# Optimization experiments

Measured on AMD Instinct MI355X. Metric: run time of the kernel, lower is better.

Reference implementation:

```python
import jax, jax.numpy as jnp
import numpy as np

B, S, H = 2, 2048, 1024
NH, NKV, HD = 16, 4, 64
G, R = NKV, NH // NKV  # 4 kv groups, 4 query heads per group


def setup_inputs() -> dict:
    key = jax.random.key(0)
    ks = jax.random.split(key, 7)
    scale = 1.0 / np.sqrt(H)
    return {
        "hidden_states": jax.random.normal(ks[0], (B, S, H), jnp.float32),
        "cos": jax.random.normal(ks[1], (S, HD), jnp.float32),
        "sin": jax.random.normal(ks[2], (S, HD), jnp.float32),
        "attention_mask": jnp.ones((B, S), jnp.float32),
        "Wq": jax.random.normal(ks[3], (H, NH * HD), jnp.float32) * scale,
        "Wk": jax.random.normal(ks[4], (H, NKV * HD), jnp.float32) * scale,
        "Wv": jax.random.normal(ks[5], (H, NKV * HD), jnp.float32) * scale,
        "Wo": jax.random.normal(ks[6], (NH * HD, H), jnp.float32) * scale,
    }


def _rotate_half(x):
    h = x.shape[-1] // 2
    return jnp.concatenate([-x[..., h:], x[..., :h]], axis=-1)


def reference(hidden_states, cos, sin, attention_mask, Wq, Wk, Wv, Wo):
    x = hidden_states
    q = (x @ Wq).reshape(B, S, NH, HD)
    k = (x @ Wk).reshape(B, S, NKV, HD)
    v = (x @ Wv).reshape(B, S, NKV, HD)
    # RoPE: cos/sin [S,HD] broadcast over batch and heads
    c = cos[None, :, None, :]
    s = sin[None, :, None, :]
    q = q * c + _rotate_half(q) * s
    k = k * c + _rotate_half(k) * s
    # GQA without materializing repeated KV: q grouped as [B,S,G,R,HD]
    qg = q.reshape(B, S, G, R, HD)
    scores = jnp.einsum("bsgrd,btgd->bgrst", qg, k) / np.sqrt(HD)  # [B,G,R,S,T]
    causal = jnp.tril(jnp.ones((S, S), bool))
    scores = jnp.where(causal[None, None, None], scores, -jnp.inf)
    scores = scores + ((1.0 - attention_mask) * -1e9)[:, None, None, None, :]
    probs = jax.nn.softmax(scores.astype(jnp.float32), axis=-1).astype(q.dtype)
    out = jnp.einsum("bgrst,btgd->bsgrd", probs, v).reshape(B, S, NH * HD)
    return out @ Wo
```

## Files before the change

kernel.cpp:

```cpp
#include <hip/hip_runtime.h>
#include <math.h>

#define B_   2
#define S_   2048
#define H_   1024
#define NH_  16
#define NKV_ 4
#define HD_  64
#define R_   (NH_ / NKV_)
#define QKVW 1536

typedef __attribute__((ext_vector_type(8))) short bf16x8;
typedef __attribute__((ext_vector_type(4))) float f32x4;

__device__ inline short f2bf(float f) {
    unsigned u = __float_as_uint(f);
    u += 0x7FFF + ((u >> 16) & 1);
    return (short)(u >> 16);
}

__device__ inline void gload_lds16(const void* gptr, void* lptr) {
    __builtin_amdgcn_global_load_lds(
        (const __attribute__((address_space(1))) unsigned int*)gptr,
        (__attribute__((address_space(3))) unsigned int*)lptr,
        16, 0, 0);
}

__global__ __launch_bounds__(256) void tconv_all(const float* __restrict__ Wq,
                                                 const float* __restrict__ Wk,
                                                 const float* __restrict__ Wv,
                                                 const float* __restrict__ Wo,
                                                 short* __restrict__ Wqkvt,
                                                 short* __restrict__ Wot) {
    __shared__ short T[64][68];
    const int bx = blockIdx.x;
    const float* W; short* Wt; int N, idx;
    if (bx < 256)      { W = Wq; Wt = Wqkvt;                     N = 1024; idx = bx; }
    else if (bx < 320) { W = Wk; Wt = Wqkvt + 1024 * 1024;       N = 256;  idx = bx - 256; }
    else if (bx < 384) { W = Wv; Wt = Wqkvt + 1280 * 1024;       N = 256;  idx = bx - 320; }
    else               { W = Wo; Wt = Wot;                       N = 1024; idx = bx - 384; }
    const int ntiles = N >> 6;
    const int n0 = (idx % ntiles) * 64;
    const int k0 = (idx / ntiles) * 64;

    const int tid = threadIdx.x;
    const int r  = tid >> 4;
    const int c4 = (tid & 15) * 4;
#pragma unroll
    for (int t = 0; t < 4; t++) {
        int row = t * 16 + r;
        float4 v = *(const float4*)&W[(size_t)(k0 + row) * N + n0 + c4];
        T[c4 + 0][row] = f2bf(v.x);
        T[c4 + 1][row] = f2bf(v.y);
        T[c4 + 2][row] = f2bf(v.z);
        T[c4 + 3][row] = f2bf(v.w);
    }
    __syncthreads();
#pragma unroll
    for (int t = 0; t < 4; t++) {
        int row = t * 16 + r;
        short4 o = *(short4*)&T[row][c4];
        *(short4*)&Wt[(size_t)(n0 + row) * 1024 + k0 + c4] = o;
    }
}

__global__ __launch_bounds__(256) void gemm1_fused(const float* __restrict__ x,
                                                   const short* __restrict__ Bt,
                                                   short* __restrict__ qkv,
                                                   short* __restrict__ Vtg,
                                                   const float* __restrict__ cosb,
                                                   const float* __restrict__ sinb) {
    __shared__ short Ah[64 * 32];
    __shared__ short Bh[128 * 32];

    const int tid  = threadIdx.x;
    const int w    = tid >> 6;
    const int lane = tid & 63;
    const int ln   = lane & 15;
    const int qd   = lane >> 4;
    const int wr   = w >> 1, wc = w & 1;
    const int row0 = blockIdx.y * 64;
    const int col0 = blockIdx.x * 128;

    const int sr = lane >> 2;
    const int sk = (lane & 3) * 8;
    const int ar  = tid >> 2;
    const int ac8 = (tid & 3) * 8;

    f32x4 acc[2][4];
#pragma unroll
    for (int mi = 0; mi < 2; mi++)
#pragma unroll
        for (int ni = 0; ni < 4; ni++)
            acc[mi][ni] = (f32x4){0.f, 0.f, 0.f, 0.f};

    for (int k0 = 0; k0 < 1024; k0 += 32) {
        __syncthreads();
        {
            const float* xp = x + (size_t)(row0 + ar) * H_ + k0 + ac8;
            float4 a = *(const float4*)xp;
            float4 b2 = *(const float4*)(xp + 4);
            bf16x8 o;
            o[0] = f2bf(a.x);  o[1] = f2bf(a.y);  o[2] = f2bf(a.z);  o[3] = f2bf(a.w);
            o[4] = f2bf(b2.x); o[5] = f2bf(b2.y); o[6] = f2bf(b2.z); o[7] = f2bf(b2.w);
            *(bf16x8*)&Ah[ar * 32 + ac8] = o;
        }
        gload_lds16(Bt + (size_t)(col0 + w * 32 + sr) * 1024 + k0 + sk, &Bh[(w * 32) * 32]);
        gload_lds16(Bt + (size_t)(col0 + w * 32 + 16 + sr) * 1024 + k0 + sk, &Bh[(w * 32 + 16) * 32]);
        __syncthreads();

        bf16x8 af[2], bfr[4];
#pragma unroll
        for (int mi = 0; mi < 2; mi++)
            af[mi] = *(const bf16x8*)&Ah[(wr * 32 + mi * 16 + ln) * 32 + qd * 8];
#pragma unroll
        for (int ni = 0; ni < 4; ni++)
            bfr[ni] = *(const bf16x8*)&Bh[(wc * 64 + ni * 16 + ln) * 32 + qd * 8];
#pragma unroll
        for (int mi = 0; mi < 2; mi++)
#pragma unroll
            for (int ni = 0; ni < 4; ni++)
                acc[mi][ni] = __builtin_amdgcn_mfma_f32_16x16x32_bf16(af[mi], bfr[ni], acc[mi][ni], 0, 0, 0);
    }

    const int colw = col0 + wc * 64;
    if (colw < H_ + NKV_ * HD_) {
#pragma unroll
        for (int mi = 0; mi < 2; mi++)
#pragma unroll
            for (int i = 0; i < 4; i++) {
                const int row  = row0 + wr * 32 + mi * 16 + qd * 4 + i;
                const int spos = row & (S_ - 1);
                const float* cp = cosb + (size_t)spos * HD_;
                const float* sp = sinb + (size_t)spos * HD_;
                float o0[4];
#pragma unroll
                for (int ni = 0; ni < 2; ni++) {
                    const int d = ni * 16 + ln;
                    float x0 = acc[mi][ni][i], x1 = acc[mi][ni + 2][i];
                    o0[ni]     = x0 * cp[d]      - x1 * sp[d];
                    o0[ni + 2] = x1 * cp[d + 32] + x0 * sp[d + 32];
                }
                short* Cp = qkv + (size_t)row * QKVW + colw + ln;
#pragma unroll
                for (int ni = 0; ni < 4; ni++) Cp[ni * 16] = f2bf(o0[ni]);
            }
    } else {
        const int g = (colw - (H_ + NKV_ * HD_)) >> 6;
#pragma unroll
        for (int mi = 0; mi < 2; mi++) {
            const int rbase = row0 + wr * 32 + mi * 16 + qd * 4;
            const int bg = ((rbase >> 11) * NKV_) + g;
            const int s0 = rbase & (S_ - 1);
#pragma unroll
            for (int ni = 0; ni < 4; ni++) {
                const int d = ni * 16 + ln;
                short4 pk = { f2bf(acc[mi][ni][0]), f2bf(acc[mi][ni][1]),
                              f2bf(acc[mi][ni][2]), f2bf(acc[mi][ni][3]) };
                *(short4*)&Vtg[((size_t)bg * HD_ + d) * S_ + s0] = pk;
            }
        }
    }
}

__global__ __launch_bounds__(256) void gemm2_bt(const short* __restrict__ A, int lda,
                                                const short* __restrict__ Bt,
                                                float* __restrict__ C, int ldc,
                                                int K) {
    __shared__ short Ah[64 * 32];
    __shared__ short Bh[128 * 32];

    const int tid  = threadIdx.x;
    const int w    = tid >> 6;
    const int lane = tid & 63;
    const int ln   = lane & 15;
    const int qd   = lane >> 4;
    const int wr   = w >> 1, wc = w & 1;
    const int row0 = blockIdx.y * 64;
    const int col0 = blockIdx.x * 128;

    const int sr = lane >> 2;
    const int sk = (lane & 3) * 8;

    f32x4 acc[2][4];
#pragma unroll
    for (int mi = 0; mi < 2; mi++)
#pragma unroll
        for (int ni = 0; ni < 4; ni++)
            acc[mi][ni] = (f32x4){0.f, 0.f, 0.f, 0.f};

    for (int k0 = 0; k0 < K; k0 += 32) {
        __syncthreads();
        gload_lds16(A + (size_t)(row0 + w * 16 + sr) * lda + k0 + sk, &Ah[(w * 16) * 32]);
        gload_lds16(Bt + (size_t)(col0 + w * 32 + sr) * K + k0 + sk, &Bh[(w * 32) * 32]);
        gload_lds16(Bt + (size_t)(col0 + w * 32 + 16 + sr) * K + k0 + sk, &Bh[(w * 32 + 16) * 32]);
        __syncthreads();

        bf16x8 af[2], bfr[4];
#pragma unroll
        for (int mi = 0; mi < 2; mi++)
            af[mi] = *(const bf16x8*)&Ah[(wr * 32 + mi * 16 + ln) * 32 + qd * 8];
#pragma unroll
        for (int ni = 0; ni < 4; ni++)
            bfr[ni] = *(const bf16x8*)&Bh[(wc * 64 + ni * 16 + ln) * 32 + qd * 8];
#pragma unroll
        for (int mi = 0; mi < 2; mi++)
#pragma unroll
            for (int ni = 0; ni < 4; ni++)
                acc[mi][ni] = __builtin_amdgcn_mfma_f32_16x16x32_bf16(af[mi], bfr[ni], acc[mi][ni], 0, 0, 0);
    }

#pragma unroll
    for (int mi = 0; mi < 2; mi++)
#pragma unroll
        for (int i = 0; i < 4; i++) {
            const size_t row = row0 + wr * 32 + mi * 16 + qd * 4 + i;
            float* Cp = C + row * ldc + col0 + wc * 64 + ln;
#pragma unroll
            for (int ni = 0; ni < 4; ni++) Cp[ni * 16] = acc[mi][ni][i];
        }
}

__global__ __launch_bounds__(256) void attn_kernel(short* __restrict__ qkv,
                                                   const short* __restrict__ Vtg,
                                                   const float* __restrict__ maskb) {
    const int tid  = threadIdx.x;
    const int w    = tid >> 6;
    const int lane = tid & 63;
    const int ln   = lane & 15;
    const int qd   = lane >> 4;

    const int fid = blockIdx.x;
    const int bg  = fid & 7;
    const int u   = fid >> 3;
    const int b   = bg >> 2;
    const int g   = bg & 3;
    const int h   = g * R_ + (u & 3);
    const int a   = u >> 2;

    __shared__ short Ps[4][32 * 72];
    short* const ps = Ps[w];

    const short* const Kb = qkv + H_ + g * HD_;

    for (int half = 0; half < 2; half++) {
        const int qt   = half ? (15 - a) : a;
        const int ws   = half ? (3 - w) : w;
        const int rowb = qt * 128 + ws * 32;
        const int nt   = (rowb >> 6) + 1;

        bf16x8 qf[2][2];
#pragma unroll
        for (int rg = 0; rg < 2; rg++) {
            const short* qp = qkv + (size_t)(b * S_ + rowb + rg * 16 + ln) * QKVW + h * HD_;
            qf[rg][0] = *(const bf16x8*)&qp[qd * 8];
            qf[rg][1] = *(const bf16x8*)&qp[32 + qd * 8];
        }

        f32x4 O[2][4] = {};
        float mrow[2] = {-1e30f, -1e30f};
        float lrow[2] = {0.0f, 0.0f};

        for (int kt = 0; kt < nt; kt++) {
            const int base = kt * 64;

            bf16x8 ka0[4], ka1[4];
#pragma unroll
            for (int kg = 0; kg < 4; kg++) {
                const short* kp = Kb + (size_t)(b * S_ + base + kg * 16 + ln) * QKVW;
                ka0[kg] = *(const bf16x8*)&kp[qd * 8];
                ka1[kg] = *(const bf16x8*)&kp[32 + qd * 8];
            }
            bf16x8 vb[2][4];
#pragma unroll
            for (int kc2 = 0; kc2 < 2; kc2++)
#pragma unroll
                for (int dt = 0; dt < 4; dt++)
                    vb[kc2][dt] = *(const bf16x8*)
                        &Vtg[((size_t)bg * HD_ + dt * 16 + ln) * S_ + base + kc2 * 32 + qd * 8];

            float mt[4][4];
#pragma unroll
            for (int kg = 0; kg < 4; kg++) {
                float4 mv = *(const float4*)&maskb[b * S_ + base + kg * 16 + qd * 4];
                mt[kg][0] = (1.0f - mv.x) * -1e9f;
                mt[kg][1] = (1.0f - mv.y) * -1e9f;
                mt[kg][2] = (1.0f - mv.z) * -1e9f;
                mt[kg][3] = (1.0f - mv.w) * -1e9f;
            }

            f32x4 St[2][4];
#pragma unroll
            for (int kg = 0; kg < 4; kg++) {
#pragma unroll
                for (int rg = 0; rg < 2; rg++) {
                    f32x4 z = {0.f, 0.f, 0.f, 0.f};
                    z = __builtin_amdgcn_mfma_f32_16x16x32_bf16(ka0[kg], qf[rg][0], z, 0, 0, 0);
                    St[rg][kg] = __builtin_amdgcn_mfma_f32_16x16x32_bf16(ka1[kg], qf[rg][1], z, 0, 0, 0);
                }
            }

            const bool diag = (kt == nt - 1);

#pragma unroll
            for (int rg = 0; rg < 2; rg++) {
                const int qrow = rowb + rg * 16 + ln;
                float sc[4][4];
#pragma unroll
                for (int kg = 0; kg < 4; kg++) {
                    const int keyb = base + kg * 16 + qd * 4;
#pragma unroll
                    for (int i = 0; i < 4; i++) {
                        float v = fmaf(St[rg][kg][i], 0.125f, mt[kg][i]);
                        sc[kg][i] = (diag && (keyb + i > qrow)) ? -1e30f : v;
                    }
                }
                float mx = sc[0][0];
#pragma unroll
                for (int kg = 0; kg < 4; kg++)
#pragma unroll
                    for (int i = 0; i < 4; i++) mx = fmaxf(mx, sc[kg][i]);
                mx = fmaxf(mx, __shfl_xor(mx, 16));
                mx = fmaxf(mx, __shfl_xor(mx, 32));

                if (__ballot(mx > mrow[rg] + 8.0f)) {
                    float nm    = fmaxf(mrow[rg], mx);
                    float alpha = __expf(mrow[rg] - nm);
                    lrow[rg] *= alpha;
#pragma unroll
                    for (int i = 0; i < 4; i++) {
                        float av = __shfl(alpha, qd * 4 + i);
#pragma unroll
                        for (int dt = 0; dt < 4; dt++) O[rg][dt][i] *= av;
                    }
                    mrow[rg] = nm;
                }
                const float nm = mrow[rg];

                float ls = 0.0f;
                float pr[4][4];
#pragma unroll
                for (int kg = 0; kg < 4; kg++)
#pragma unroll
                    for (int i = 0; i < 4; i++) {
                        float p = __expf(sc[kg][i] - nm);
                        pr[kg][i] = p;
                        ls += p;
                    }
                ls += __shfl_xor(ls, 16);
                ls += __shfl_xor(ls, 32);
                lrow[rg] += ls;

#pragma unroll
                for (int kg = 0; kg < 4; kg++) {
                    short4 pk = { f2bf(pr[kg][0]), f2bf(pr[kg][1]),
                                  f2bf(pr[kg][2]), f2bf(pr[kg][3]) };
                    *(short4*)&ps[(rg * 16 + ln) * 72 + kg * 16 + qd * 4] = pk;
                }
            }

#pragma unroll
            for (int kc2 = 0; kc2 < 2; kc2++) {
                bf16x8 pa0 = *(const bf16x8*)&ps[(ln)      * 72 + kc2 * 32 + qd * 8];
                bf16x8 pa1 = *(const bf16x8*)&ps[(16 + ln) * 72 + kc2 * 32 + qd * 8];
#pragma unroll
                for (int dt = 0; dt < 4; dt++) {
                    O[0][dt] = __builtin_amdgcn_mfma_f32_16x16x32_bf16(pa0, vb[kc2][dt], O[0][dt], 0, 0, 0);
                    O[1][dt] = __builtin_amdgcn_mfma_f32_16x16x32_bf16(pa1, vb[kc2][dt], O[1][dt], 0, 0, 0);
                }
            }
        }

#pragma unroll
        for (int rg = 0; rg < 2; rg++)
#pragma unroll
            for (int i = 0; i < 4; i++) {
                float li  = __shfl(lrow[rg], qd * 4 + i);
                float inv = 1.0f / li;
                const int row = rowb + rg * 16 + qd * 4 + i;
                short* op = qkv + (size_t)(b * S_ + row) * QKVW + h * HD_ + ln;
#pragma unroll
                for (int dt = 0; dt < 4; dt++) op[dt * 16] = f2bf(O[rg][dt][i] * inv);
            }
    }
}

extern "C" void kernel_launch(void* const* d_in, const int* in_sizes, int n_in,
                              void* d_out, int out_size, void* d_ws, size_t ws_size,
                              hipStream_t stream) {
    const float* x     = (const float*)d_in[0];
    const float* cosb  = (const float*)d_in[1];
    const float* sinb  = (const float*)d_in[2];
    const float* maskb = (const float*)d_in[3];
    const float* Wq    = (const float*)d_in[4];
    const float* Wk    = (const float*)d_in[5];
    const float* Wv    = (const float*)d_in[6];
    const float* Wo    = (const float*)d_in[7];

    const int M = B_ * S_;

    short* qkv   = (short*)d_ws;
    short* Wqkvt = qkv + (size_t)M * QKVW;
    short* Wot   = Wqkvt + (size_t)QKVW * H_;
    short* Vtg   = Wot + (size_t)H_ * H_;
    float* out   = (float*)d_out;

    dim3 blk(256);

    tconv_all<<<dim3(640), blk, 0, stream>>>(Wq, Wk, Wv, Wo, Wqkvt, Wot);

    gemm1_fused<<<dim3(QKVW / 128, M / 64), blk, 0, stream>>>(x, Wqkvt, qkv, Vtg, cosb, sinb);

    attn_kernel<<<dim3(256), blk, 0, stream>>>(qkv, Vtg, maskb);

    gemm2_bt<<<dim3(H_ / 128, M / 64), blk, 0, stream>>>(qkv, QKVW, Wot, out, H_, H_);
}
```

Before: 204.3 us.

## Split attention into 16-row query strips with double-buffered KV prefetch

Each wave now owns a 16-row query strip instead of 32 rows. The launch grows to 512 blocks with launch_bounds(256,2), so more waves are in flight and causal work is balanced by pairing strip j with strip 127-j. The K and V fragments for the next tile are loaded into a second register set while the current tile is computed, which hides global-load latency. The cost is that each loaded K/V tile is reused by half as many query rows, roughly doubling K/V traffic, and the double buffers add register pressure.

```diff
diff --git a/kernel.cpp b/kernel.cpp
--- a/kernel.cpp
+++ b/kernel.cpp
@@ -221,9 +221,9 @@
         }
 }
 
-__global__ __launch_bounds__(256) void attn_kernel(short* __restrict__ qkv,
-                                                   const short* __restrict__ Vtg,
-                                                   const float* __restrict__ maskb) {
+__global__ __launch_bounds__(256, 2) void attn_kernel(short* __restrict__ qkv,
+                                                      const short* __restrict__ Vtg,
+                                                      const float* __restrict__ maskb) {
     const int tid  = threadIdx.x;
     const int w    = tid >> 6;
     const int lane = tid & 63;
@@ -236,152 +236,163 @@
     const int b   = bg >> 2;
     const int g   = bg & 3;
     const int h   = g * R_ + (u & 3);
-    const int a   = u >> 2;
-
-    __shared__ short Ps[4][32 * 72];
+    const int t   = u >> 2;
+    const int j0  = t * 4 + w;
+
+    __shared__ short Ps[4][16 * 72];
     short* const ps = Ps[w];
 
-    const short* const Kb = qkv + H_ + g * HD_;
-
-    for (int half = 0; half < 2; half++) {
-        const int qt   = half ? (15 - a) : a;
-        const int ws   = half ? (3 - w) : w;
-        const int rowb = qt * 128 + ws * 32;
-        const int nt   = (rowb >> 6) + 1;
-
-        bf16x8 qf[2][2];
-#pragma unroll
-        for (int rg = 0; rg < 2; rg++) {
-            const short* qp = qkv + (size_t)(b * S_ + rowb + rg * 16 + ln) * QKVW + h * HD_;
-            qf[rg][0] = *(const bf16x8*)&qp[qd * 8];
-            qf[rg][1] = *(const bf16x8*)&qp[32 + qd * 8];
-        }
-
-        f32x4 O[2][4] = {};
-        float mrow[2] = {-1e30f, -1e30f};
-        float lrow[2] = {0.0f, 0.0f};
-
-        for (int kt = 0; kt < nt; kt++) {
-            const int base = kt * 64;
-
-            bf16x8 ka0[4], ka1[4];
+    const short* const Kb = qkv + (size_t)b * S_ * QKVW + H_ + g * HD_;
+    const short* const Vb = Vtg + (size_t)bg * HD_ * S_;
+    const float* const mb = maskb + b * S_;
+
+#pragma unroll 1
+    for (int ss = 0; ss < 2; ss++) {
+        const int j    = ss ? (127 - j0) : j0;
+        const int rowb = j * 16;
+        const int nt   = (j >> 2) + 1;
+
+        bf16x8 qf0, qf1;
+        {
+            const short* qp = qkv + (size_t)(b * S_ + rowb + ln) * QKVW + h * HD_;
+            qf0 = *(const bf16x8*)&qp[qd * 8];
+            qf1 = *(const bf16x8*)&qp[32 + qd * 8];
+        }
+
+        f32x4 O[4] = {};
+        float mrow = -1e30f;
+        float lrow = 0.0f;
+
+        bf16x8 kaA0[4], kaA1[4], vbA[2][4];
+        bf16x8 kaB0[4], kaB1[4], vbB[2][4];
+
+        auto load_kv = [&](bf16x8 (&ka0)[4], bf16x8 (&ka1)[4], bf16x8 (&vb)[2][4],
+                           int base) {
 #pragma unroll
             for (int kg = 0; kg < 4; kg++) {
-                const short* kp = Kb + (size_t)(b * S_ + base + kg * 16 + ln) * QKVW;
+                const short* kp = Kb + (size_t)(base + kg * 16 + ln) * QKVW;
                 ka0[kg] = *(const bf16x8*)&kp[qd * 8];
                 ka1[kg] = *(const bf16x8*)&kp[32 + qd * 8];
             }
-            bf16x8 vb[2][4];
 #pragma unroll
             for (int kc2 = 0; kc2 < 2; kc2++)
 #pragma unroll
                 for (int dt = 0; dt < 4; dt++)
                     vb[kc2][dt] = *(const bf16x8*)
-                        &Vtg[((size_t)bg * HD_ + dt * 16 + ln) * S_ + base + kc2 * 32 + qd * 8];
+                        &Vb[(size_t)(dt * 16 + ln) * S_ + base + kc2 * 32 + qd * 8];
+        };
+
+        auto tile = [&](const bf16x8 (&ka0)[4], const bf16x8 (&ka1)[4],
+                        const bf16x8 (&vb)[2][4], int kt) {
+            const int base = kt * 64;
 
             float mt[4][4];
 #pragma unroll
             for (int kg = 0; kg < 4; kg++) {
-                float4 mv = *(const float4*)&maskb[b * S_ + base + kg * 16 + qd * 4];
+                float4 mv = *(const float4*)&mb[base + kg * 16 + qd * 4];
                 mt[kg][0] = (1.0f - mv.x) * -1e9f;
                 mt[kg][1] = (1.0f - mv.y) * -1e9f;
                 mt[kg][2] = (1.0f - mv.z) * -1e9f;
                 mt[kg][3] = (1.0f - mv.w) * -1e9f;
             }
 
-            f32x4 St[2][4];
+            f32x4 St[4];
 #pragma unroll
             for (int kg = 0; kg < 4; kg++) {
-#pragma unroll
-                for (int rg = 0; rg < 2; rg++) {
-                    f32x4 z = {0.f, 0.f, 0.f, 0.f};
-                    z = __builtin_amdgcn_mfma_f32_16x16x32_bf16(ka0[kg], qf[rg][0], z, 0, 0, 0);
-                    St[rg][kg] = __builtin_amdgcn_mfma_f32_16x16x32_bf16(ka1[kg], qf[rg][1], z, 0, 0, 0);
+                f32x4 z = {0.f, 0.f, 0.f, 0.f};
+                z = __builtin_amdgcn_mfma_f32_16x16x32_bf16(ka0[kg], qf0, z, 0, 0, 0);
+                St[kg] = __builtin_amdgcn_mfma_f32_16x16x32_bf16(ka1[kg], qf1, z, 0, 0, 0);
+            }
+
+            const bool diag = (kt == nt - 1);
+            const int qrow  = rowb + ln;
+
+            float sc[4][4];
+#pragma unroll
+            for (int kg = 0; kg < 4; kg++) {
+                const int keyb = base + kg * 16 + qd * 4;
+#pragma unroll
+                for (int i = 0; i < 4; i++) {
+                    float v = fmaf(St[kg][i], 0.125f, mt[kg][i]);
+                    sc[kg][i] = (diag && (keyb + i > qrow)) ? -1e30f : v;
                 }
             }
-
-            const bool diag = (kt == nt - 1);
-
-#pragma unroll
-            for (int rg = 0; rg < 2; rg++) {
-                const int qrow = rowb + rg * 16 + ln;
-                float sc[4][4];
-#pragma unroll
-                for (int kg = 0; kg < 4; kg++) {
-                    const int keyb = base + kg * 16 + qd * 4;
-#pragma unroll
-                    for (int i = 0; i < 4; i++) {
-                        float v = fmaf(St[rg][kg][i], 0.125f, mt[kg][i]);
-                        sc[kg][i] = (diag && (keyb + i > qrow)) ? -1e30f : v;
-                    }
+            float mx = sc[0][0];
+#pragma unroll
+            for (int kg = 0; kg < 4; kg++)
+#pragma unroll
+                for (int i = 0; i < 4; i++) mx = fmaxf(mx, sc[kg][i]);
+            mx = fmaxf(mx, __shfl_xor(mx, 16));
+            mx = fmaxf(mx, __shfl_xor(mx, 32));
+
+            if (__ballot(mx > mrow + 8.0f)) {
+                float nm    = fmaxf(mrow, mx);
+                float alpha = __expf(mrow - nm);
+                lrow *= alpha;
+#pragma unroll
+                for (int i = 0; i < 4; i++) {
+                    float av = __shfl(alpha, qd * 4 + i);
+#pragma unroll
+                    for (int dt = 0; dt < 4; dt++) O[dt][i] *= av;
                 }
-                float mx = sc[0][0];
-#pragma unroll
-                for (int kg = 0; kg < 4; kg++)
-#pragma unroll
-                    for (int i = 0; i < 4; i++) mx = fmaxf(mx, sc[kg][i]);
-                mx = fmaxf(mx, __shfl_xor(mx, 16));
-                mx = fmaxf(mx, __shfl_xor(mx, 32));
-
-                if (__ballot(mx > mrow[rg] + 8.0f)) {
-                    float nm    = fmaxf(mrow[rg], mx);
-                    float alpha = __expf(mrow[rg] - nm);
-                    lrow[rg] *= alpha;
-#pragma unroll
-                    for (int i = 0; i < 4; i++) {
-                        float av = __shfl(alpha, qd * 4 + i);
-#pragma unroll
-                        for (int dt = 0; dt < 4; dt++) O[rg][dt][i] *= av;
-                    }
-                    mrow[rg] = nm;
+                mrow = nm;
+            }
+            const float nm = mrow;
+
+            float ls = 0.0f;
+            float pr[4][4];
+#pragma unroll
+            for (int kg = 0; kg < 4; kg++)
+#pragma unroll
+                for (int i = 0; i < 4; i++) {
+                    float p = __expf(sc[kg][i] - nm);
+                    pr[kg][i] = p;
+                    ls += p;
                 }
-                const float nm = mrow[rg];
-
-                float ls = 0.0f;
-                float pr[4][4];
-#pragma unroll
-                for (int kg = 0; kg < 4; kg++)
-#pragma unroll
-                    for (int i = 0; i < 4; i++) {
-                        float p = __expf(sc[kg][i] - nm);
-                        pr[kg][i] = p;
-                        ls += p;
-                    }
-                ls += __shfl_xor(ls, 16);
-                ls += __shfl_xor(ls, 32);
-                lrow[rg] += ls;
-
-#pragma unroll
-                for (int kg = 0; kg < 4; kg++) {
-                    short4 pk = { f2bf(pr[kg][0]), f2bf(pr[kg][1]),
-                                  f2bf(pr[kg][2]), f2bf(pr[kg][3]) };
-                    *(short4*)&ps[(rg * 16 + ln) * 72 + kg * 16 + qd * 4] = pk;
-                }
+            ls += __shfl_xor(ls, 16);
+            ls += __shfl_xor(ls, 32);
+            lrow += ls;
+
+#pragma unroll
+            for (int kg = 0; kg < 4; kg++) {
+                short4 pk = { f2bf(pr[kg][0]), f2bf(pr[kg][1]),
+                              f2bf(pr[kg][2]), f2bf(pr[kg][3]) };
+                *(short4*)&ps[ln * 72 + kg * 16 + qd * 4] = pk;
             }
 
 #pragma unroll
             for (int kc2 = 0; kc2 < 2; kc2++) {
-                bf16x8 pa0 = *(const bf16x8*)&ps[(ln)      * 72 + kc2 * 32 + qd * 8];
-                bf16x8 pa1 = *(const bf16x8*)&ps[(16 + ln) * 72 + kc2 * 32 + qd * 8];
-#pragma unroll
-                for (int dt = 0; dt < 4; dt++) {
-                    O[0][dt] = __builtin_amdgcn_mfma_f32_16x16x32_bf16(pa0, vb[kc2][dt], O[0][dt], 0, 0, 0);
-                    O[1][dt] = __builtin_amdgcn_mfma_f32_16x16x32_bf16(pa1, vb[kc2][dt], O[1][dt], 0, 0, 0);
-                }
-            }
-        }
-
-#pragma unroll
-        for (int rg = 0; rg < 2; rg++)
-#pragma unroll
-            for (int i = 0; i < 4; i++) {
-                float li  = __shfl(lrow[rg], qd * 4 + i);
-                float inv = 1.0f / li;
-                const int row = rowb + rg * 16 + qd * 4 + i;
-                short* op = qkv + (size_t)(b * S_ + row) * QKVW + h * HD_ + ln;
-#pragma unroll
-                for (int dt = 0; dt < 4; dt++) op[dt * 16] = f2bf(O[rg][dt][i] * inv);
-            }
+                bf16x8 pa = *(const bf16x8*)&ps[ln * 72 + kc2 * 32 + qd * 8];
+#pragma unroll
+                for (int dt = 0; dt < 4; dt++)
+                    O[dt] = __builtin_amdgcn_mfma_f32_16x16x32_bf16(pa, vb[kc2][dt], O[dt], 0, 0, 0);
+            }
+        };
+
+        load_kv(kaA0, kaA1, vbA, 0);
+        int kt = 0;
+        while (true) {
+            bool pf = (kt + 1 < nt);
+            if (pf) load_kv(kaB0, kaB1, vbB, (kt + 1) * 64);
+            tile(kaA0, kaA1, vbA, kt);
+            kt++;
+            if (!pf) break;
+            pf = (kt + 1 < nt);
+            if (pf) load_kv(kaA0, kaA1, vbA, (kt + 1) * 64);
+            tile(kaB0, kaB1, vbB, kt);
+            kt++;
+            if (!pf) break;
+        }
+
+#pragma unroll
+        for (int i = 0; i < 4; i++) {
+            float li  = __shfl(lrow, qd * 4 + i);
+            float inv = 1.0f / li;
+            const int row = rowb + qd * 4 + i;
+            short* op = qkv + (size_t)(b * S_ + row) * QKVW + h * HD_ + ln;
+#pragma unroll
+            for (int dt = 0; dt < 4; dt++) op[dt * 16] = f2bf(O[dt][i] * inv);
+        }
     }
 }
 
@@ -411,7 +422,7 @@
 
     gemm1_fused<<<dim3(QKVW / 128, M / 64), blk, 0, stream>>>(x, Wqkvt, qkv, Vtg, cosb, sinb);
 
-    attn_kernel<<<dim3(256), blk, 0, stream>>>(qkv, Vtg, maskb);
+    attn_kernel<<<dim3(512), blk, 0, stream>>>(qkv, Vtg, maskb);
 
     gemm2_bt<<<dim3(H_ / 128, M / 64), blk, 0, stream>>>(qkv, QKVW, Wot, out, H_, H_);
 }
```

New measurement: 289.0 us. +41.5%, slower.

## Share K/V tiles in LDS across 8 waves with double-buffered prefetch in attention

Applied to the files above, without the earlier changes.

The attention kernel now runs 512 threads per block, with both causal halves (q tile a and 15-a) processed at once by separate waves instead of sequentially. K, V and mask tiles are loaded cooperatively into double-buffered shared memory with a register prefetch of the next tile, replacing per-wave direct global loads. The aim is to cut redundant global/L2 traffic and overlap loads with compute. In exchange it adds a block-wide barrier per key tile, and waves whose causal range has ended sit idle while still joining the loop.

```diff
diff --git a/kernel.cpp b/kernel.cpp
--- a/kernel.cpp
+++ b/kernel.cpp
@@ -221,9 +221,9 @@
         }
 }
 
-__global__ __launch_bounds__(256) void attn_kernel(short* __restrict__ qkv,
-                                                   const short* __restrict__ Vtg,
-                                                   const float* __restrict__ maskb) {
+__global__ __launch_bounds__(512, 2) void attn_kernel(short* __restrict__ qkv,
+                                                      const short* __restrict__ Vtg,
+                                                      const float* __restrict__ maskb) {
     const int tid  = threadIdx.x;
     const int w    = tid >> 6;
     const int lane = tid & 63;
@@ -238,69 +238,88 @@
     const int h   = g * R_ + (u & 3);
     const int a   = u >> 2;
 
-    __shared__ short Ps[4][32 * 72];
+    const int qt   = (w < 4) ? a : (15 - a);
+    const int st   = w & 3;
+    const int rowb = qt * 128 + st * 32;
+    const int ktd  = 2 * qt + (st >> 1);
+    const int nt   = 32 - 2 * a;
+
+    __shared__ short Ks[2][64 * 72];
+    __shared__ short Vt[2][64 * 72];
+    __shared__ short Ps[8][16 * 72];
+    __shared__ float mskS[2][64];
     short* const ps = Ps[w];
 
-    const short* const Kb = qkv + H_ + g * HD_;
-
-    for (int half = 0; half < 2; half++) {
-        const int qt   = half ? (15 - a) : a;
-        const int ws   = half ? (3 - w) : w;
-        const int rowb = qt * 128 + ws * 32;
-        const int nt   = (rowb >> 6) + 1;
-
-        bf16x8 qf[2][2];
-#pragma unroll
-        for (int rg = 0; rg < 2; rg++) {
-            const short* qp = qkv + (size_t)(b * S_ + rowb + rg * 16 + ln) * QKVW + h * HD_;
-            qf[rg][0] = *(const bf16x8*)&qp[qd * 8];
-            qf[rg][1] = *(const bf16x8*)&qp[32 + qd * 8];
-        }
-
-        f32x4 O[2][4] = {};
-        float mrow[2] = {-1e30f, -1e30f};
-        float lrow[2] = {0.0f, 0.0f};
-
-        for (int kt = 0; kt < nt; kt++) {
-            const int base = kt * 64;
-
-            bf16x8 ka0[4], ka1[4];
+    const short* const Kb = qkv + (size_t)b * S_ * QKVW + H_ + g * HD_;
+    const short* const Vb = Vtg + (size_t)bg * HD_ * S_;
+    const float* const mb = maskb + b * S_;
+
+    const int fr = tid >> 3;
+    const int fc = (tid & 7) * 8;
+
+    bf16x8 qf[2][2];
+#pragma unroll
+    for (int rg = 0; rg < 2; rg++) {
+        const short* qp = qkv + (size_t)(b * S_ + rowb + rg * 16 + ln) * QKVW + h * HD_;
+        qf[rg][0] = *(const bf16x8*)&qp[qd * 8];
+        qf[rg][1] = *(const bf16x8*)&qp[32 + qd * 8];
+    }
+
+    f32x4 O[2][4] = {};
+    float mrow[2] = {-1e30f, -1e30f};
+    float lrow[2] = {0.0f, 0.0f};
+
+    *(bf16x8*)&Ks[0][fr * 72 + fc] = *(const bf16x8*)&Kb[(size_t)fr * QKVW + fc];
+    *(bf16x8*)&Vt[0][fr * 72 + fc] = *(const bf16x8*)&Vb[(size_t)fr * S_ + fc];
+    if (tid < 64) mskS[0][tid] = mb[tid];
+    __syncthreads();
+
+    int cur = 0;
+    for (int kt = 0; kt < nt; kt++) {
+        const int base = kt * 64;
+        const bool pf = (kt + 1 < nt);
+
+        bf16x8 pk, pv;
+        float pm = 0.0f;
+        if (pf) {
+            const int nb = base + 64;
+            pk = *(const bf16x8*)&Kb[(size_t)(nb + fr) * QKVW + fc];
+            pv = *(const bf16x8*)&Vb[(size_t)fr * S_ + nb + fc];
+            if (tid < 64) pm = mb[nb + tid];
+        }
+
+        if (kt <= ktd) {
+            f32x4 St[2][4];
 #pragma unroll
             for (int kg = 0; kg < 4; kg++) {
-                const short* kp = Kb + (size_t)(b * S_ + base + kg * 16 + ln) * QKVW;
-                ka0[kg] = *(const bf16x8*)&kp[qd * 8];
-                ka1[kg] = *(const bf16x8*)&kp[32 + qd * 8];
+                bf16x8 ka0 = *(const bf16x8*)&Ks[cur][(kg * 16 + ln) * 72 + qd * 8];
+                bf16x8 ka1 = *(const bf16x8*)&Ks[cur][(kg * 16 + ln) * 72 + 32 + qd * 8];
+#pragma unroll
+                for (int rg = 0; rg < 2; rg++) {
+                    f32x4 z = {0.f, 0.f, 0.f, 0.f};
+                    z = __builtin_amdgcn_mfma_f32_16x16x32_bf16(ka0, qf[rg][0], z, 0, 0, 0);
+                    St[rg][kg] = __builtin_amdgcn_mfma_f32_16x16x32_bf16(ka1, qf[rg][1], z, 0, 0, 0);
+                }
             }
+
             bf16x8 vb[2][4];
 #pragma unroll
             for (int kc2 = 0; kc2 < 2; kc2++)
 #pragma unroll
                 for (int dt = 0; dt < 4; dt++)
-                    vb[kc2][dt] = *(const bf16x8*)
-                        &Vtg[((size_t)bg * HD_ + dt * 16 + ln) * S_ + base + kc2 * 32 + qd * 8];
+                    vb[kc2][dt] = *(const bf16x8*)&Vt[cur][(dt * 16 + ln) * 72 + kc2 * 32 + qd * 8];
 
             float mt[4][4];
 #pragma unroll
             for (int kg = 0; kg < 4; kg++) {
-                float4 mv = *(const float4*)&maskb[b * S_ + base + kg * 16 + qd * 4];
+                float4 mv = *(const float4*)&mskS[cur][kg * 16 + qd * 4];
                 mt[kg][0] = (1.0f - mv.x) * -1e9f;
                 mt[kg][1] = (1.0f - mv.y) * -1e9f;
                 mt[kg][2] = (1.0f - mv.z) * -1e9f;
                 mt[kg][3] = (1.0f - mv.w) * -1e9f;
             }
 
-            f32x4 St[2][4];
-#pragma unroll
-            for (int kg = 0; kg < 4; kg++) {
-#pragma unroll
-                for (int rg = 0; rg < 2; rg++) {
-                    f32x4 z = {0.f, 0.f, 0.f, 0.f};
-                    z = __builtin_amdgcn_mfma_f32_16x16x32_bf16(ka0[kg], qf[rg][0], z, 0, 0, 0);
-                    St[rg][kg] = __builtin_amdgcn_mfma_f32_16x16x32_bf16(ka1[kg], qf[rg][1], z, 0, 0, 0);
-                }
-            }
-
-            const bool diag = (kt == nt - 1);
+            const bool diag = (kt == ktd);
 
 #pragma unroll
             for (int rg = 0; rg < 2; rg++) {
@@ -338,13 +357,12 @@
                 const float nm = mrow[rg];
 
                 float ls = 0.0f;
-                float pr[4][4];
 #pragma unroll
                 for (int kg = 0; kg < 4; kg++)
 #pragma unroll
                     for (int i = 0; i < 4; i++) {
                         float p = __expf(sc[kg][i] - nm);
-                        pr[kg][i] = p;
+                        sc[kg][i] = p;
                         ls += p;
                     }
                 ls += __shfl_xor(ls, 16);
@@ -353,36 +371,42 @@
 
 #pragma unroll
                 for (int kg = 0; kg < 4; kg++) {
-                    short4 pk = { f2bf(pr[kg][0]), f2bf(pr[kg][1]),
-                                  f2bf(pr[kg][2]), f2bf(pr[kg][3]) };
-                    *(short4*)&ps[(rg * 16 + ln) * 72 + kg * 16 + qd * 4] = pk;
+                    short4 pk2 = { f2bf(sc[kg][0]), f2bf(sc[kg][1]),
+                                   f2bf(sc[kg][2]), f2bf(sc[kg][3]) };
+                    *(short4*)&ps[ln * 72 + kg * 16 + qd * 4] = pk2;
+                }
+
+#pragma unroll
+                for (int kc2 = 0; kc2 < 2; kc2++) {
+                    bf16x8 pa = *(const bf16x8*)&ps[ln * 72 + kc2 * 32 + qd * 8];
+#pragma unroll
+                    for (int dt = 0; dt < 4; dt++)
+                        O[rg][dt] = __builtin_amdgcn_mfma_f32_16x16x32_bf16(pa, vb[kc2][dt], O[rg][dt], 0, 0, 0);
                 }
             }
-
-#pragma unroll
-            for (int kc2 = 0; kc2 < 2; kc2++) {
-                bf16x8 pa0 = *(const bf16x8*)&ps[(ln)      * 72 + kc2 * 32 + qd * 8];
-                bf16x8 pa1 = *(const bf16x8*)&ps[(16 + ln) * 72 + kc2 * 32 + qd * 8];
-#pragma unroll
-                for (int dt = 0; dt < 4; dt++) {
-                    O[0][dt] = __builtin_amdgcn_mfma_f32_16x16x32_bf16(pa0, vb[kc2][dt], O[0][dt], 0, 0, 0);
-                    O[1][dt] = __builtin_amdgcn_mfma_f32_16x16x32_bf16(pa1, vb[kc2][dt], O[1][dt], 0, 0, 0);
-                }
-            }
-        }
-
-#pragma unroll
-        for (int rg = 0; rg < 2; rg++)
-#pragma unroll
-            for (int i = 0; i < 4; i++) {
-                float li  = __shfl(lrow[rg], qd * 4 + i);
-                float inv = 1.0f / li;
-                const int row = rowb + rg * 16 + qd * 4 + i;
-                short* op = qkv + (size_t)(b * S_ + row) * QKVW + h * HD_ + ln;
-#pragma unroll
-                for (int dt = 0; dt < 4; dt++) op[dt * 16] = f2bf(O[rg][dt][i] * inv);
-            }
-    }
+        }
+
+        if (pf) {
+            const int nxt = cur ^ 1;
+            *(bf16x8*)&Ks[nxt][fr * 72 + fc] = pk;
+            *(bf16x8*)&Vt[nxt][fr * 72 + fc] = pv;
+            if (tid < 64) mskS[nxt][tid] = pm;
+        }
+        __syncthreads();
+        cur ^= 1;
+    }
+
+#pragma unroll
+    for (int rg = 0; rg < 2; rg++)
+#pragma unroll
+        for (int i = 0; i < 4; i++) {
+            float li  = __shfl(lrow[rg], qd * 4 + i);
+            float inv = 1.0f / li;
+            const int row = rowb + rg * 16 + qd * 4 + i;
+            short* op = qkv + (size_t)(b * S_ + row) * QKVW + h * HD_ + ln;
+#pragma unroll
+            for (int dt = 0; dt < 4; dt++) op[dt * 16] = f2bf(O[rg][dt][i] * inv);
+        }
 }
 
 extern "C" void kernel_launch(void* const* d_in, const int* in_sizes, int n_in,
@@ -411,7 +435,7 @@
 
     gemm1_fused<<<dim3(QKVW / 128, M / 64), blk, 0, stream>>>(x, Wqkvt, qkv, Vtg, cosb, sinb);
 
-    attn_kernel<<<dim3(256), blk, 0, stream>>>(qkv, Vtg, maskb);
+    attn_kernel<<<dim3(256), dim3(512), 0, stream>>>(qkv, Vtg, maskb);
 
     gemm2_bt<<<dim3(H_ / 128, M / 64), blk, 0, stream>>>(qkv, QKVW, Wot, out, H_, H_);
 }
```

Result: no change. 201.0 us (-1.6%).
